# Kernel tuning notes

Hardware: AMD Instinct MI355X
Metric: run time of the kernel (lower is better)

## Reference

```python
import jax, jax.numpy as jnp
import numpy as np

M, N, K, C, G = 16384, 131072, 16, 128, 8
EPS_BN = 1e-5


def _bn(x, g, b):
    # inference-mode BatchNorm1d (running_mean=0, running_var=1)
    return x * (g / jnp.sqrt(1.0 + EPS_BN)) + b


def setup_inputs() -> dict:
    key = jax.random.key(0)
    ks = jax.random.split(key, 16)
    f32 = jnp.float32
    s = 0.05
    return {
        "query_feat": jax.random.normal(ks[0], (M, C), f32),
        "context_feat": jax.random.normal(ks[1], (N, C), f32),
        "query_coord": jax.random.normal(ks[2], (M, 3), f32),
        "context_coord": jax.random.normal(ks[3], (N, 3), f32),
        "Wq": jax.random.normal(ks[4], (C, C), f32) * s,
        "bq": jnp.zeros((C,), f32),
        "gq": jnp.ones((C,), f32),
        "betaq": jnp.zeros((C,), f32),
        "Wk": jax.random.normal(ks[5], (C, C), f32) * s,
        "bk": jnp.zeros((C,), f32),
        "gk": jnp.ones((C,), f32),
        "betak": jnp.zeros((C,), f32),
        "Wv": jax.random.normal(ks[6], (C, C), f32) * s,
        "bv": jnp.zeros((C,), f32),
        "Wp1": jax.random.normal(ks[7], (3, C), f32) * s,
        "bp1": jnp.zeros((C,), f32),
        "gp1": jnp.ones((C,), f32),
        "betap1": jnp.zeros((C,), f32),
        "Wp2": jax.random.normal(ks[8], (C, C), f32) * s,
        "bp2": jnp.zeros((C,), f32),
        "Ww1": jax.random.normal(ks[9], (C, G), f32) * s,
        "bw1": jnp.zeros((G,), f32),
        "gw1": jnp.ones((G,), f32),
        "betaw1": jnp.zeros((G,), f32),
        "Ww2": jax.random.normal(ks[10], (G, G), f32) * s,
        "bw2": jnp.zeros((G,), f32),
        "knn_indexes": jax.random.randint(ks[11], (M, K), 0, N, dtype=jnp.int32),
    }


def reference(query_feat, context_feat, query_coord, context_coord,
              Wq, bq, gq, betaq, Wk, bk, gk, betak, Wv, bv,
              Wp1, bp1, gp1, betap1, Wp2, bp2,
              Ww1, bw1, gw1, betaw1, Ww2, bw2, knn_indexes):
    q = jax.nn.relu(_bn(query_feat @ Wq + bq, gq, betaq))              # (M, C)
    k = jax.nn.relu(_bn(context_feat @ Wk + bk, gk, betak))            # (N, C)
    v = context_feat @ Wv + bv                                         # (N, C)

    mask = knn_indexes >= 0                                            # (M, K); -1 = padded neighbor
    idx = jnp.where(mask, knn_indexes, 0)
    mf = mask[..., None].astype(q.dtype)                               # (M, K, 1)

    key_g = k[idx] * mf                                                # (M, K, C) gather (zero row for -1)
    val_g = v[idx] * mf                                                # (M, K, C)
    pos = (context_coord[idx] - query_coord[:, None, :]) * mf          # (M, K, 3) relative position

    # positional-encoding bias branch (pe_bias=True, pe_multiplier=False)
    peb = jax.nn.relu(_bn(pos @ Wp1 + bp1, gp1, betap1)) @ Wp2 + bp2   # (M, K, C)
    rel = key_g - q[:, None, :] + peb                                  # (M, K, C)
    val_g = val_g + peb

    # grouped vector attention weights
    w = jax.nn.relu(_bn(rel @ Ww1 + bw1, gw1, betaw1)) @ Ww2 + bw2     # (M, K, G)
    w = jax.nn.softmax(w, axis=1) * mf                                 # softmax over neighbors, mask padded

    m_, k_ = idx.shape
    c_ = q.shape[-1]
    g_ = w.shape[-1]
    out = jnp.einsum('mkgi,mkg->mgi', val_g.reshape(m_, k_, g_, c_ // g_), w)
    return out.reshape(m_, c_)
```

## Files before the change

kernel.cpp:

```cpp
#include <hip/hip_runtime.h>

#define C 128
#define G 8
#define KNN 16
#define QB 4
#define EPS 1e-5f

typedef unsigned short u16;
typedef __attribute__((ext_vector_type(8))) short short8;
typedef __attribute__((ext_vector_type(4))) float float4v;

union frag_u { short8 v; u16 u[8]; unsigned d[4]; };

__device__ inline u16 f2bf(float f) {
    unsigned u = __builtin_bit_cast(unsigned, f);
    unsigned r = (u + 0x7fffu + ((u >> 16) & 1u)) >> 16;
    return (u16)r;
}
__device__ inline float bf2f(u16 h) {
    unsigned u = ((unsigned)h) << 16;
    return __builtin_bit_cast(float, u);
}
__device__ inline unsigned pk2(float lo, float hi) {
    unsigned r;
    asm("v_cvt_pk_bf16_f32 %0, %1, %2" : "=v"(r) : "v"(lo), "v"(hi));
    return r;
}
__device__ inline u16 f2bf1(float f) { return (u16)pk2(f, f); }
__device__ inline float bflo(unsigned v) { return __builtin_bit_cast(float, v << 16); }
__device__ inline float bfhi(unsigned v) { return __builtin_bit_cast(float, v & 0xffff0000u); }

__global__ __launch_bounds__(256) void prep_w(
    const float* __restrict__ Wk, const float* __restrict__ Wv,
    const float* __restrict__ Wq, const float* __restrict__ Wp2,
    const float* __restrict__ Ww1, const float* __restrict__ bp2,
    u16* __restrict__ dst, float* __restrict__ cw1)
{
    __shared__ float w1s[C * G];
    const int b = blockIdx.x, t = threadIdx.x;
    if (b < 16) {
        const int mi = b >> 2, qt = b & 3;
        const float* W = mi == 0 ? Wk : mi == 1 ? Wv : mi == 2 ? Wq : Wp2;
        u16* d = dst + mi * 16384;
        for (int e = qt * 4096 + t; e < (qt + 1) * 4096; e += 256) {
            const int k = e >> 7, n = e & 127;
            const int cb = n >> 4, lan = n & 15;
            const int kk = k >> 5, quad = (k >> 3) & 3, j = k & 7;
            d[(((cb * 4 + kk) * 4 + quad) * 16 + lan) * 8 + j] = f2bf(W[e]);
        }
    } else if (b == 16) {
        u16* d = dst + 4 * 16384;
        for (int e = t; e < 4096; e += 256) {
            const int j = e & 7, lan = (e >> 3) & 15;
            const int quad = (e >> 7) & 3, kk = e >> 9;
            const int k = kk * 32 + quad * 8 + j;
            d[e] = lan < 8 ? f2bf(Ww1[k * G + lan]) : (u16)0;
        }
    } else {
        u16* d = dst + 4 * 16384 + 4096;
        for (int e = t; e < 4096; e += 256) d[e] = 0;
        for (int e = t; e < C * G; e += 256) w1s[e] = Ww1[e];
        __syncthreads();
#pragma unroll
        for (int it = 0; it < 4; it++) {
            const int k = it * 32 + (t >> 3), g = t & 7;
            const float4* Wr = (const float4*)(Wp2 + k * C);
            float a = 0.f;
#pragma unroll 8
            for (int i4 = 0; i4 < 32; i4++) {
                const float4 wv = Wr[i4];
                a = fmaf(wv.x, w1s[(i4 * 4 + 0) * G + g], a);
                a = fmaf(wv.y, w1s[(i4 * 4 + 1) * G + g], a);
                a = fmaf(wv.z, w1s[(i4 * 4 + 2) * G + g], a);
                a = fmaf(wv.w, w1s[(i4 * 4 + 3) * G + g], a);
            }
            const int kk = k >> 5, quad = (k >> 3) & 3, j = k & 7;
            d[((kk * 4 + quad) * 16 + g) * 8 + j] = f2bf(a);
        }
        if (t < G) {
            float a = 0.f;
#pragma unroll 8
            for (int i = 0; i < C; i++) a = fmaf(bp2[i], w1s[i * G + t], a);
            cw1[t] = a;
        }
    }
}

__global__ __launch_bounds__(256) void proj_all(
    const float* __restrict__ Xc, const float* __restrict__ Xq,
    const u16* __restrict__ PWk, const float* __restrict__ bk,
    const float* __restrict__ gk, const float* __restrict__ betak,
    const u16* __restrict__ PWv, const float* __restrict__ bv,
    const u16* __restrict__ PWq, const float* __restrict__ bq,
    const float* __restrict__ gq, const float* __restrict__ betaq,
    const u16* __restrict__ PWw1b,
    u16* __restrict__ vout, u16* __restrict__ Kp, u16* __restrict__ Qp,
    int nkv)
{
    __shared__ u16 Xs[64 * 136];
    const int t = threadIdx.x;
    const int w = t >> 6, l = t & 63;
    const int quad = l >> 4, lan = l & 15;
    const bool isq = (int)blockIdx.x >= nkv;
    const long long row0 = (long long)(isq ? blockIdx.x - nkv : blockIdx.x) * 64;
    const float* X = isq ? Xq : Xc;

    {
        const float4* Xv = (const float4*)(X + row0 * C);
#pragma unroll
        for (int i = 0; i < 8; i++) {
            const int e = t + 256 * i;
            const int r = e >> 5, c4 = e & 31;
            const float4 f = Xv[e];
            uint2 p;
            p.x = pk2(f.x, f.y);
            p.y = pk2(f.z, f.w);
            *(uint2*)(&Xs[r * 136 + c4 * 4]) = p;
        }
    }
    __syncthreads();

    if (!isq) {
        unsigned vp[2][4][2];
        {
            short8 Bf[2][4];
#pragma unroll
            for (int ct = 0; ct < 2; ct++) {
                const int cb = w * 2 + ct;
#pragma unroll
                for (int kk = 0; kk < 4; kk++)
                    Bf[ct][kk] = *(const short8*)(PWv + (((cb * 4 + kk) * 4 + quad) * 16 + lan) * 8);
            }
            const float b0v = bv[w * 32 + lan], b1v = bv[w * 32 + 16 + lan];
            float4v acc[2][4];
#pragma unroll
            for (int rt = 0; rt < 4; rt++) {
                acc[0][rt] = (float4v)b0v;
                acc[1][rt] = (float4v)b1v;
            }
#pragma unroll
            for (int rt = 0; rt < 4; rt++)
#pragma unroll
                for (int kk = 0; kk < 4; kk++) {
                    const short8 A = *(const short8*)(&Xs[(rt * 16 + lan) * 136 + kk * 32 + quad * 8]);
#pragma unroll
                    for (int ct = 0; ct < 2; ct++)
                        acc[ct][rt] = __builtin_amdgcn_mfma_f32_16x16x32_bf16(
                            A, Bf[ct][kk], acc[ct][rt], 0, 0, 0);
                }
#pragma unroll
            for (int ct = 0; ct < 2; ct++)
#pragma unroll
                for (int rt = 0; rt < 4; rt++)
#pragma unroll
                    for (int h = 0; h < 2; h++)
                        vp[ct][rt][h] = pk2(acc[ct][rt][2 * h], acc[ct][rt][2 * h + 1]);
        }
        float4v acck[2][4];
        {
            short8 Bf[2][4];
#pragma unroll
            for (int ct = 0; ct < 2; ct++) {
                const int cb = w * 2 + ct;
#pragma unroll
                for (int kk = 0; kk < 4; kk++)
                    Bf[ct][kk] = *(const short8*)(PWk + (((cb * 4 + kk) * 4 + quad) * 16 + lan) * 8);
            }
            const float b0k = bk[w * 32 + lan], b1k = bk[w * 32 + 16 + lan];
#pragma unroll
            for (int rt = 0; rt < 4; rt++) {
                acck[0][rt] = (float4v)b0k;
                acck[1][rt] = (float4v)b1k;
            }
#pragma unroll
            for (int rt = 0; rt < 4; rt++)
#pragma unroll
                for (int kk = 0; kk < 4; kk++) {
                    const short8 A = *(const short8*)(&Xs[(rt * 16 + lan) * 136 + kk * 32 + quad * 8]);
#pragma unroll
                    for (int ct = 0; ct < 2; ct++)
                        acck[ct][rt] = __builtin_amdgcn_mfma_f32_16x16x32_bf16(
                            A, Bf[ct][kk], acck[ct][rt], 0, 0, 0);
                }
        }
        __syncthreads();

#pragma unroll
        for (int ct = 0; ct < 2; ct++) {
            const int cg = w * 32 + ct * 16 + lan;
            const float sc = gk[cg] * rsqrtf(1.f + EPS);
            const float sh = betak[cg];
#pragma unroll
            for (int rt = 0; rt < 4; rt++)
#pragma unroll
                for (int reg = 0; reg < 4; reg++) {
                    float y = fmaf(acck[ct][rt][reg], sc, sh);
                    y = y > 0.f ? y : 0.f;
                    Xs[(rt * 16 + quad * 4 + reg) * 136 + cg] = f2bf1(y);
                }
        }
        __syncthreads();

        {
            short8 Bw[4];
#pragma unroll
            for (int kk = 0; kk < 4; kk++)
                Bw[kk] = *(const short8*)(PWw1b + ((kk * 4 + quad) * 16 + lan) * 8);
            float4v ka = (float4v)0.f;
#pragma unroll
            for (int kk = 0; kk < 4; kk++) {
                const short8 A = *(const short8*)(&Xs[(w * 16 + lan) * 136 + kk * 32 + quad * 8]);
                ka = __builtin_amdgcn_mfma_f32_16x16x32_bf16(A, Bw[kk], ka, 0, 0, 0);
            }
            if (lan < G) {
#pragma unroll
                for (int reg = 0; reg < 4; reg++)
                    Kp[(row0 + w * 16 + quad * 4 + reg) * G + lan] = f2bf1(ka[reg]);
            }
        }
        __syncthreads();

#pragma unroll
        for (int ct = 0; ct < 2; ct++) {
            const int cg = w * 32 + ct * 16 + lan;
#pragma unroll
            for (int rt = 0; rt < 4; rt++)
#pragma unroll
                for (int h = 0; h < 2; h++) {
                    Xs[(rt * 16 + quad * 4 + 2 * h) * 136 + cg]     = (u16)(vp[ct][rt][h] & 0xffffu);
                    Xs[(rt * 16 + quad * 4 + 2 * h + 1) * 136 + cg] = (u16)(vp[ct][rt][h] >> 16);
                }
        }
        __syncthreads();
#pragma unroll
        for (int i = 0; i < 4; i++) {
            const int e = t + 256 * i;
            const int r = e >> 4, cc = (e & 15) * 8;
            *(short8*)(vout + (row0 + r) * C + cc) = *(const short8*)(&Xs[r * 136 + cc]);
        }
    } else {
        float4v acc[2][4];
        {
            short8 Bf[2][4];
#pragma unroll
            for (int ct = 0; ct < 2; ct++) {
                const int cb = w * 2 + ct;
#pragma unroll
                for (int kk = 0; kk < 4; kk++)
                    Bf[ct][kk] = *(const short8*)(PWq + (((cb * 4 + kk) * 4 + quad) * 16 + lan) * 8);
            }
            const float b0q = bq[w * 32 + lan], b1q = bq[w * 32 + 16 + lan];
#pragma unroll
            for (int rt = 0; rt < 4; rt++) {
                acc[0][rt] = (float4v)b0q;
                acc[1][rt] = (float4v)b1q;
            }
#pragma unroll
            for (int rt = 0; rt < 4; rt++)
#pragma unroll
                for (int kk = 0; kk < 4; kk++) {
                    const short8 A = *(const short8*)(&Xs[(rt * 16 + lan) * 136 + kk * 32 + quad * 8]);
#pragma unroll
                    for (int ct = 0; ct < 2; ct++)
                        acc[ct][rt] = __builtin_amdgcn_mfma_f32_16x16x32_bf16(
                            A, Bf[ct][kk], acc[ct][rt], 0, 0, 0);
                }
        }
        __syncthreads();
#pragma unroll
        for (int ct = 0; ct < 2; ct++) {
            const int cg = w * 32 + ct * 16 + lan;
            const float sc = gq[cg] * rsqrtf(1.f + EPS);
            const float sh = betaq[cg];
#pragma unroll
            for (int rt = 0; rt < 4; rt++)
#pragma unroll
                for (int reg = 0; reg < 4; reg++) {
                    float y = fmaf(acc[ct][rt][reg], sc, sh);
                    y = y > 0.f ? y : 0.f;
                    Xs[(rt * 16 + quad * 4 + reg) * 136 + cg] = f2bf1(y);
                }
        }
        __syncthreads();
        {
            short8 Bw[4];
#pragma unroll
            for (int kk = 0; kk < 4; kk++)
                Bw[kk] = *(const short8*)(PWw1b + ((kk * 4 + quad) * 16 + lan) * 8);
            float4v qa = (float4v)0.f;
#pragma unroll
            for (int kk = 0; kk < 4; kk++) {
                const short8 A = *(const short8*)(&Xs[(w * 16 + lan) * 136 + kk * 32 + quad * 8]);
                qa = __builtin_amdgcn_mfma_f32_16x16x32_bf16(A, Bw[kk], qa, 0, 0, 0);
            }
            if (lan < G) {
#pragma unroll
                for (int reg = 0; reg < 4; reg++)
                    Qp[(row0 + w * 16 + quad * 4 + reg) * G + lan] = f2bf1(qa[reg]);
            }
        }
    }
}

__global__ __launch_bounds__(256) void attn6(
    const u16* __restrict__ vbuf, const u16* __restrict__ Kp,
    const u16* __restrict__ Qp,
    const float* __restrict__ qcoord, const float* __restrict__ ccoord,
    const float* __restrict__ Wp1, const float* __restrict__ bp1,
    const float* __restrict__ gp1, const float* __restrict__ betap1,
    const u16* __restrict__ PWp2, const float* __restrict__ bp2,
    const u16* __restrict__ PWp2pb, const float* __restrict__ cw1,
    const float* __restrict__ bw1,
    const float* __restrict__ gw1, const float* __restrict__ betaw1,
    const float* __restrict__ Ww2, const float* __restrict__ bw2,
    const int* __restrict__ knn, float* __restrict__ out)
{
    __shared__ u16   fA[64 * 136];
    __shared__ u16   kgs[64 * G];
    __shared__ float qps[QB * G];
    __shared__ float pebp[64 * G];
    __shared__ float cw1s[G];
    __shared__ float ww2s[G * G];
    __shared__ float pxs[64], pys[64], pzs[64];
    __shared__ int   idxs[64];
    __shared__ float wl[QB * 16 * G];

    const int t = threadIdx.x;
    const int w = t >> 6, l = t & 63;
    const int quad = l >> 4, lan = l & 15;
    const int m0 = blockIdx.x * QB;
    const int rsub = t >> 4;
    const int c8 = (t & 15) * 8;

    float mfr[4];
    frag_u vg[4];
#pragma unroll
    for (int p = 0; p < 4; p++) {
        const int ii = knn[m0 * KNN + p * 16 + rsub];
        mfr[p] = ii >= 0 ? 1.f : 0.f;
        const size_t i0 = ii >= 0 ? ii : 0;
        vg[p].v = *(const short8*)(vbuf + i0 * C + c8);
    }
    if (t < 64) {
        const int q = t >> 4;
        const int ii = knn[m0 * KNN + t];
        const float mf = ii >= 0 ? 1.f : 0.f;
        const int i0 = ii >= 0 ? ii : 0;
        idxs[t] = ii;
        pxs[t] = (ccoord[i0 * 3 + 0] - qcoord[(m0 + q) * 3 + 0]) * mf;
        pys[t] = (ccoord[i0 * 3 + 1] - qcoord[(m0 + q) * 3 + 1]) * mf;
        pzs[t] = (ccoord[i0 * 3 + 2] - qcoord[(m0 + q) * 3 + 2]) * mf;
        *(short8*)(&kgs[t * G]) = *(const short8*)(Kp + (size_t)i0 * G);
    } else if (t < 68) {
        const int p = t - 64;
        frag_u qv;
        qv.v = *(const short8*)(Qp + (size_t)(m0 + p) * G);
#pragma unroll
        for (int j = 0; j < G; j++) qps[p * G + j] = bf2f(qv.u[j]);
    } else if (t < 76) {
        cw1s[t - 68] = cw1[t - 68];
    } else if (t < 76 + G * G) {
        ww2s[t - 76] = Ww2[t - 76];
    }
    __syncthreads();

    {
        const int pc = t & 63;
        const int c0 = 2 * pc;
        const float2 g2  = *(const float2*)(&gp1[c0]);
        const float2 b2  = *(const float2*)(&bp1[c0]);
        const float2 be2 = *(const float2*)(&betap1[c0]);
        const float2 wr0 = *(const float2*)(&Wp1[c0]);
        const float2 wr1 = *(const float2*)(&Wp1[C + c0]);
        const float2 wr2 = *(const float2*)(&Wp1[2 * C + c0]);
        const float rsq = rsqrtf(1.f + EPS);
        const float sc0 = g2.x * rsq, sc1 = g2.y * rsq;
        const float w00 = wr0.x * sc0, w01 = wr0.y * sc1;
        const float w10 = wr1.x * sc0, w11 = wr1.y * sc1;
        const float w20 = wr2.x * sc0, w21 = wr2.y * sc1;
        const float bb0 = fmaf(b2.x, sc0, be2.x);
        const float bb1 = fmaf(b2.y, sc1, be2.y);
#pragma unroll
        for (int r2 = 0; r2 < 16; r2++) {
            const int r = w * 16 + r2;
            const float x = pxs[r], y = pys[r], z = pzs[r];
            float ya = fmaf(x, w00, fmaf(y, w10, fmaf(z, w20, bb0)));
            float yb = fmaf(x, w01, fmaf(y, w11, fmaf(z, w21, bb1)));
            ya = ya > 0.f ? ya : 0.f;
            yb = yb > 0.f ? yb : 0.f;
            *(unsigned*)(&fA[r * 136 + c0]) = pk2(ya, yb);
        }
    }
    __syncthreads();

    float4v acc[2][4];
    float4v pp = (float4v)0.f;
    {
        short8 Bf[2][4];
#pragma unroll
        for (int ct = 0; ct < 2; ct++) {
            const int cb = w * 2 + ct;
#pragma unroll
            for (int kk = 0; kk < 4; kk++)
                Bf[ct][kk] = *(const short8*)(PWp2 + (((cb * 4 + kk) * 4 + quad) * 16 + lan) * 8);
        }
        const float b0 = bp2[w * 32 + lan], b1 = bp2[w * 32 + 16 + lan];
#pragma unroll
        for (int q = 0; q < 4; q++) {
            acc[0][q] = (float4v)b0;
            acc[1][q] = (float4v)b1;
        }
#pragma unroll
        for (int q = 0; q < 4; q++)
#pragma unroll
            for (int kk = 0; kk < 4; kk++) {
                const short8 A = *(const short8*)(&fA[(q * 16 + lan) * 136 + kk * 32 + quad * 8]);
#pragma unroll
                for (int ct = 0; ct < 2; ct++)
                    acc[ct][q] = __builtin_amdgcn_mfma_f32_16x16x32_bf16(
                        A, Bf[ct][kk], acc[ct][q], 0, 0, 0);
            }
#pragma unroll
        for (int kk = 0; kk < 4; kk++) {
            const short8 Bp = *(const short8*)(PWp2pb + ((kk * 4 + quad) * 16 + lan) * 8);
            const short8 A = *(const short8*)(&fA[(w * 16 + lan) * 136 + kk * 32 + quad * 8]);
            pp = __builtin_amdgcn_mfma_f32_16x16x32_bf16(A, Bp, pp, 0, 0, 0);
        }
    }
    __syncthreads();

    {
#pragma unroll
        for (int ct = 0; ct < 2; ct++)
#pragma unroll
            for (int q = 0; q < 4; q++)
#pragma unroll
                for (int reg = 0; reg < 4; reg++)
                    fA[(q * 16 + quad * 4 + reg) * 136 + w * 32 + ct * 16 + lan] =
                        f2bf1(acc[ct][q][reg]);
        if (lan < G) {
#pragma unroll
            for (int reg = 0; reg < 4; reg++)
                pebp[(w * 16 + quad * 4 + reg) * G + lan] = pp[reg];
        }
    }
    __syncthreads();

    {
#pragma unroll
        for (int p = 0; p < 4; p++) {
            const int r = p * 16 + rsub;
            const float mf = mfr[p];
            frag_u peb, o;
            peb.v = *(const short8*)(&fA[r * 136 + c8]);
#pragma unroll
            for (int dd = 0; dd < 4; dd++) {
                const unsigned pv = peb.d[dd], vv = vg[p].d[dd];
                o.d[dd] = pk2(fmaf(bflo(vv), mf, bflo(pv)),
                              fmaf(bfhi(vv), mf, bfhi(pv)));
            }
            *(short8*)(&fA[r * 136 + c8]) = o.v;
        }
    }
    {
        const int j = l & 15;
        const int r = (w << 4) + j;
        const float mf = idxs[r] >= 0 ? 1.f : 0.f;
        const int g0 = 2 * quad, g1 = g0 + 1;
        const float L0 = bf2f(kgs[r * G + g0]) * mf - qps[w * G + g0]
                       + pebp[r * G + g0] + cw1s[g0] + bw1[g0];
        const float L1 = bf2f(kgs[r * G + g1]) * mf - qps[w * G + g1]
                       + pebp[r * G + g1] + cw1s[g1] + bw1[g1];
        const float y0 = L0 * (gw1[g0] * rsqrtf(1.f + EPS)) + betaw1[g0];
        const float y1 = L1 * (gw1[g1] * rsqrtf(1.f + EPS)) + betaw1[g1];
        wl[w * 128 + j * 8 + g0] = y0 > 0.f ? y0 : 0.f;
        wl[w * 128 + j * 8 + g1] = y1 > 0.f ? y1 : 0.f;
    }
    __syncthreads();

    {
        const int j = l & 15;
        const int g0 = 2 * quad, g1 = g0 + 1;
        float hw_[8];
#pragma unroll
        for (int g = 0; g < 8; g++) hw_[g] = wl[w * 128 + j * 8 + g];
        float a0 = bw2[g0], a1 = bw2[g1];
#pragma unroll
        for (int g = 0; g < 8; g++) {
            a0 = fmaf(hw_[g], ww2s[g * 8 + g0], a0);
            a1 = fmaf(hw_[g], ww2s[g * 8 + g1], a1);
        }
        float mx0 = a0, mx1 = a1;
#pragma unroll
        for (int off = 1; off < 16; off <<= 1) {
            mx0 = fmaxf(mx0, __shfl_xor(mx0, off));
            mx1 = fmaxf(mx1, __shfl_xor(mx1, off));
        }
        const float e0 = __expf(a0 - mx0), e1 = __expf(a1 - mx1);
        float s0 = e0, s1 = e1;
#pragma unroll
        for (int off = 1; off < 16; off <<= 1) {
            s0 += __shfl_xor(s0, off);
            s1 += __shfl_xor(s1, off);
        }
        const float mf = idxs[(w << 4) + j] >= 0 ? 1.f : 0.f;
        wl[w * 128 + j * 8 + g0] = e0 * (1.f / s0) * mf;
        wl[w * 128 + j * 8 + g1] = e1 * (1.f / s1) * mf;
    }
    __syncthreads();

    {
        const int q = t >> 6;
        const int pc = t & 63;
        const int c0 = 2 * pc;
        const int g = pc >> 3;
        float s0 = 0.f, s1 = 0.f;
#pragma unroll
        for (int j = 0; j < KNN; j++) {
            const unsigned v = *(const unsigned*)(&fA[(q * 16 + j) * 136 + c0]);
            const float wv = wl[q * 128 + j * 8 + g];
            s0 = fmaf(bflo(v), wv, s0);
            s1 = fmaf(bfhi(v), wv, s1);
        }
        *(float2*)(&out[(size_t)(m0 + q) * C + c0]) = make_float2(s0, s1);
    }
}

extern "C" void kernel_launch(void* const* d_in, const int* in_sizes, int n_in,
                              void* d_out, int out_size, void* d_ws, size_t ws_size,
                              hipStream_t stream)
{
    const float* query_feat    = (const float*)d_in[0];
    const float* context_feat  = (const float*)d_in[1];
    const float* query_coord   = (const float*)d_in[2];
    const float* context_coord = (const float*)d_in[3];
    const float* Wq    = (const float*)d_in[4];
    const float* bq    = (const float*)d_in[5];
    const float* gq    = (const float*)d_in[6];
    const float* betaq = (const float*)d_in[7];
    const float* Wk    = (const float*)d_in[8];
    const float* bk    = (const float*)d_in[9];
    const float* gk    = (const float*)d_in[10];
    const float* betak = (const float*)d_in[11];
    const float* Wv    = (const float*)d_in[12];
    const float* bv    = (const float*)d_in[13];
    const float* Wp1   = (const float*)d_in[14];
    const float* bp1   = (const float*)d_in[15];
    const float* gp1   = (const float*)d_in[16];
    const float* betap1= (const float*)d_in[17];
    const float* Wp2   = (const float*)d_in[18];
    const float* bp2   = (const float*)d_in[19];
    const float* Ww1   = (const float*)d_in[20];
    const float* bw1   = (const float*)d_in[21];
    const float* gw1   = (const float*)d_in[22];
    const float* betaw1= (const float*)d_in[23];
    const float* Ww2   = (const float*)d_in[24];
    const float* bw2   = (const float*)d_in[25];
    const int*   knn   = (const int*)d_in[26];

    const int M = in_sizes[0] / C;
    const int N = in_sizes[1] / C;

    u16* vb = (u16*)d_ws;
    u16* Kp = vb + (size_t)N * C;
    u16* Qp = Kp + (size_t)N * G;
    u16* pw = Qp + (size_t)M * G;
    u16* pWk    = pw;
    u16* pWv    = pw + 16384;
    u16* pWq    = pw + 2 * 16384;
    u16* pWp2   = pw + 3 * 16384;
    u16* pWw1b  = pw + 4 * 16384;
    u16* pWp2pb = pw + 4 * 16384 + 4096;
    float* cw1  = (float*)(pw + 4 * 16384 + 2 * 4096);

    prep_w<<<18, 256, 0, stream>>>(Wk, Wv, Wq, Wp2, Ww1, bp2, pw, cw1);
    proj_all<<<N / 64 + M / 64, 256, 0, stream>>>(
        context_feat, query_feat,
        pWk, bk, gk, betak, pWv, bv,
        pWq, bq, gq, betaq, pWw1b,
        vb, Kp, Qp, N / 64);
    attn6<<<M / QB, 256, 0, stream>>>(vb, Kp, Qp, query_coord, context_coord,
                                      Wp1, bp1, gp1, betap1, pWp2, bp2,
                                      pWp2pb, cw1, bw1, gw1, betaw1, Ww2, bw2,
                                      knn, (float*)d_out);
}
```

Before: 209.8 us.

## Process eight queries per attention block and pack relative positions as float4

```diff
diff --git a/kernel.cpp b/kernel.cpp
--- a/kernel.cpp
+++ b/kernel.cpp
@@ -3,7 +3,7 @@
 #define C 128
 #define G 8
 #define KNN 16
-#define QB 4
+#define QB 8
 #define EPS 1e-5f
 
 typedef unsigned short u16;
@@ -315,14 +315,14 @@
     const float* __restrict__ Ww2, const float* __restrict__ bw2,
     const int* __restrict__ knn, float* __restrict__ out)
 {
-    __shared__ u16   fA[64 * 136];
-    __shared__ u16   kgs[64 * G];
+    __shared__ u16   fA[128 * 136];
+    __shared__ u16   kgs[128 * G];
     __shared__ float qps[QB * G];
-    __shared__ float pebp[64 * G];
+    __shared__ float pebp[128 * G];
     __shared__ float cw1s[G];
     __shared__ float ww2s[G * G];
-    __shared__ float pxs[64], pys[64], pzs[64];
-    __shared__ int   idxs[64];
+    __shared__ float4 ps4[128];
+    __shared__ int   idxs[128];
     __shared__ float wl[QB * 16 * G];
 
     const int t = threadIdx.x;
@@ -332,35 +332,38 @@
     const int rsub = t >> 4;
     const int c8 = (t & 15) * 8;
 
-    float mfr[4];
-    frag_u vg[4];
-#pragma unroll
-    for (int p = 0; p < 4; p++) {
+    float mfr[8];
+    frag_u vg[8];
+#pragma unroll
+    for (int p = 0; p < 8; p++) {
         const int ii = knn[m0 * KNN + p * 16 + rsub];
         mfr[p] = ii >= 0 ? 1.f : 0.f;
         const size_t i0 = ii >= 0 ? ii : 0;
         vg[p].v = *(const short8*)(vbuf + i0 * C + c8);
     }
-    if (t < 64) {
+    if (t < 128) {
         const int q = t >> 4;
         const int ii = knn[m0 * KNN + t];
         const float mf = ii >= 0 ? 1.f : 0.f;
         const int i0 = ii >= 0 ? ii : 0;
         idxs[t] = ii;
-        pxs[t] = (ccoord[i0 * 3 + 0] - qcoord[(m0 + q) * 3 + 0]) * mf;
-        pys[t] = (ccoord[i0 * 3 + 1] - qcoord[(m0 + q) * 3 + 1]) * mf;
-        pzs[t] = (ccoord[i0 * 3 + 2] - qcoord[(m0 + q) * 3 + 2]) * mf;
+        float4 p4;
+        p4.x = (ccoord[i0 * 3 + 0] - qcoord[(m0 + q) * 3 + 0]) * mf;
+        p4.y = (ccoord[i0 * 3 + 1] - qcoord[(m0 + q) * 3 + 1]) * mf;
+        p4.z = (ccoord[i0 * 3 + 2] - qcoord[(m0 + q) * 3 + 2]) * mf;
+        p4.w = 0.f;
+        ps4[t] = p4;
         *(short8*)(&kgs[t * G]) = *(const short8*)(Kp + (size_t)i0 * G);
-    } else if (t < 68) {
-        const int p = t - 64;
+    } else if (t < 128 + QB) {
+        const int p = t - 128;
         frag_u qv;
         qv.v = *(const short8*)(Qp + (size_t)(m0 + p) * G);
 #pragma unroll
         for (int j = 0; j < G; j++) qps[p * G + j] = bf2f(qv.u[j]);
-    } else if (t < 76) {
-        cw1s[t - 68] = cw1[t - 68];
-    } else if (t < 76 + G * G) {
-        ww2s[t - 76] = Ww2[t - 76];
+    } else if (t < 136 + G) {
+        cw1s[t - 136] = cw1[t - 136];
+    } else if (t < 144 + G * G) {
+        ww2s[t - 144] = Ww2[t - 144];
     }
     __syncthreads();
 
@@ -381,11 +384,11 @@
         const float bb0 = fmaf(b2.x, sc0, be2.x);
         const float bb1 = fmaf(b2.y, sc1, be2.y);
 #pragma unroll
-        for (int r2 = 0; r2 < 16; r2++) {
-            const int r = w * 16 + r2;
-            const float x = pxs[r], y = pys[r], z = pzs[r];
-            float ya = fmaf(x, w00, fmaf(y, w10, fmaf(z, w20, bb0)));
-            float yb = fmaf(x, w01, fmaf(y, w11, fmaf(z, w21, bb1)));
+        for (int r2 = 0; r2 < 32; r2++) {
+            const int r = w * 32 + r2;
+            const float4 p4 = ps4[r];
+            float ya = fmaf(p4.x, w00, fmaf(p4.y, w10, fmaf(p4.z, w20, bb0)));
+            float yb = fmaf(p4.x, w01, fmaf(p4.y, w11, fmaf(p4.z, w21, bb1)));
             ya = ya > 0.f ? ya : 0.f;
             yb = yb > 0.f ? yb : 0.f;
             *(unsigned*)(&fA[r * 136 + c0]) = pk2(ya, yb);
@@ -393,8 +396,8 @@
     }
     __syncthreads();
 
-    float4v acc[2][4];
-    float4v pp = (float4v)0.f;
+    float4v acc[2][8];
+    float4v pp0 = (float4v)0.f, pp1 = (float4v)0.f;
     {
         short8 Bf[2][4];
 #pragma unroll
@@ -406,12 +409,12 @@
         }
         const float b0 = bp2[w * 32 + lan], b1 = bp2[w * 32 + 16 + lan];
 #pragma unroll
-        for (int q = 0; q < 4; q++) {
+        for (int q = 0; q < 8; q++) {
             acc[0][q] = (float4v)b0;
             acc[1][q] = (float4v)b1;
         }
 #pragma unroll
-        for (int q = 0; q < 4; q++)
+        for (int q = 0; q < 8; q++)
 #pragma unroll
             for (int kk = 0; kk < 4; kk++) {
                 const short8 A = *(const short8*)(&fA[(q * 16 + lan) * 136 + kk * 32 + quad * 8]);
@@ -420,11 +423,16 @@
                     acc[ct][q] = __builtin_amdgcn_mfma_f32_16x16x32_bf16(
                         A, Bf[ct][kk], acc[ct][q], 0, 0, 0);
             }
+        short8 Bp[4];
+#pragma unroll
+        for (int kk = 0; kk < 4; kk++)
+            Bp[kk] = *(const short8*)(PWp2pb + ((kk * 4 + quad) * 16 + lan) * 8);
 #pragma unroll
         for (int kk = 0; kk < 4; kk++) {
-            const short8 Bp = *(const short8*)(PWp2pb + ((kk * 4 + quad) * 16 + lan) * 8);
-            const short8 A = *(const short8*)(&fA[(w * 16 + lan) * 136 + kk * 32 + quad * 8]);
-            pp = __builtin_amdgcn_mfma_f32_16x16x32_bf16(A, Bp, pp, 0, 0, 0);
+            const short8 A0 = *(const short8*)(&fA[(w * 16 + lan) * 136 + kk * 32 + quad * 8]);
+            pp0 = __builtin_amdgcn_mfma_f32_16x16x32_bf16(A0, Bp[kk], pp0, 0, 0, 0);
+            const short8 A1 = *(const short8*)(&fA[((w + 4) * 16 + lan) * 136 + kk * 32 + quad * 8]);
+            pp1 = __builtin_amdgcn_mfma_f32_16x16x32_bf16(A1, Bp[kk], pp1, 0, 0, 0);
         }
     }
     __syncthreads();
@@ -433,22 +441,24 @@
 #pragma unroll
         for (int ct = 0; ct < 2; ct++)
 #pragma unroll
-            for (int q = 0; q < 4; q++)
+            for (int q = 0; q < 8; q++)
 #pragma unroll
                 for (int reg = 0; reg < 4; reg++)
                     fA[(q * 16 + quad * 4 + reg) * 136 + w * 32 + ct * 16 + lan] =
                         f2bf1(acc[ct][q][reg]);
         if (lan < G) {
 #pragma unroll
-            for (int reg = 0; reg < 4; reg++)
-                pebp[(w * 16 + quad * 4 + reg) * G + lan] = pp[reg];
+            for (int reg = 0; reg < 4; reg++) {
+                pebp[(w * 16 + quad * 4 + reg) * G + lan] = pp0[reg];
+                pebp[((w + 4) * 16 + quad * 4 + reg) * G + lan] = pp1[reg];
+            }
         }
     }
     __syncthreads();
 
     {
 #pragma unroll
-        for (int p = 0; p < 4; p++) {
+        for (int p = 0; p < 8; p++) {
             const int r = p * 16 + rsub;
             const float mf = mfr[p];
             frag_u peb, o;
@@ -464,65 +474,79 @@
     }
     {
         const int j = l & 15;
-        const int r = (w << 4) + j;
-        const float mf = idxs[r] >= 0 ? 1.f : 0.f;
         const int g0 = 2 * quad, g1 = g0 + 1;
-        const float L0 = bf2f(kgs[r * G + g0]) * mf - qps[w * G + g0]
-                       + pebp[r * G + g0] + cw1s[g0] + bw1[g0];
-        const float L1 = bf2f(kgs[r * G + g1]) * mf - qps[w * G + g1]
-                       + pebp[r * G + g1] + cw1s[g1] + bw1[g1];
-        const float y0 = L0 * (gw1[g0] * rsqrtf(1.f + EPS)) + betaw1[g0];
-        const float y1 = L1 * (gw1[g1] * rsqrtf(1.f + EPS)) + betaw1[g1];
-        wl[w * 128 + j * 8 + g0] = y0 > 0.f ? y0 : 0.f;
-        wl[w * 128 + j * 8 + g1] = y1 > 0.f ? y1 : 0.f;
+        const float scw0 = gw1[g0] * rsqrtf(1.f + EPS);
+        const float scw1 = gw1[g1] * rsqrtf(1.f + EPS);
+#pragma unroll
+        for (int qq = 0; qq < 2; qq++) {
+            const int q = 4 * qq + w;
+            const int r = (q << 4) + j;
+            const float mf = idxs[r] >= 0 ? 1.f : 0.f;
+            const float L0 = bf2f(kgs[r * G + g0]) * mf - qps[q * G + g0]
+                           + pebp[r * G + g0] + cw1s[g0] + bw1[g0];
+            const float L1 = bf2f(kgs[r * G + g1]) * mf - qps[q * G + g1]
+                           + pebp[r * G + g1] + cw1s[g1] + bw1[g1];
+            const float y0 = L0 * scw0 + betaw1[g0];
+            const float y1 = L1 * scw1 + betaw1[g1];
+            wl[q * 128 + j * 8 + g0] = y0 > 0.f ? y0 : 0.f;
+            wl[q * 128 + j * 8 + g1] = y1 > 0.f ? y1 : 0.f;
+        }
     }
     __syncthreads();
 
     {
         const int j = l & 15;
         const int g0 = 2 * quad, g1 = g0 + 1;
-        float hw_[8];
-#pragma unroll
-        for (int g = 0; g < 8; g++) hw_[g] = wl[w * 128 + j * 8 + g];
-        float a0 = bw2[g0], a1 = bw2[g1];
-#pragma unroll
-        for (int g = 0; g < 8; g++) {
-            a0 = fmaf(hw_[g], ww2s[g * 8 + g0], a0);
-            a1 = fmaf(hw_[g], ww2s[g * 8 + g1], a1);
-        }
-        float mx0 = a0, mx1 = a1;
-#pragma unroll
-        for (int off = 1; off < 16; off <<= 1) {
-            mx0 = fmaxf(mx0, __shfl_xor(mx0, off));
-            mx1 = fmaxf(mx1, __shfl_xor(mx1, off));
-        }
-        const float e0 = __expf(a0 - mx0), e1 = __expf(a1 - mx1);
-        float s0 = e0, s1 = e1;
-#pragma unroll
-        for (int off = 1; off < 16; off <<= 1) {
-            s0 += __shfl_xor(s0, off);
-            s1 += __shfl_xor(s1, off);
-        }
-        const float mf = idxs[(w << 4) + j] >= 0 ? 1.f : 0.f;
-        wl[w * 128 + j * 8 + g0] = e0 * (1.f / s0) * mf;
-        wl[w * 128 + j * 8 + g1] = e1 * (1.f / s1) * mf;
+        const float bb0 = bw2[g0], bb1 = bw2[g1];
+#pragma unroll
+        for (int qq = 0; qq < 2; qq++) {
+            const int q = 4 * qq + w;
+            float hw_[8];
+#pragma unroll
+            for (int g = 0; g < 8; g++) hw_[g] = wl[q * 128 + j * 8 + g];
+            float a0 = bb0, a1 = bb1;
+#pragma unroll
+            for (int g = 0; g < 8; g++) {
+                a0 = fmaf(hw_[g], ww2s[g * 8 + g0], a0);
+                a1 = fmaf(hw_[g], ww2s[g * 8 + g1], a1);
+            }
+            float mx0 = a0, mx1 = a1;
+#pragma unroll
+            for (int off = 1; off < 16; off <<= 1) {
+                mx0 = fmaxf(mx0, __shfl_xor(mx0, off));
+                mx1 = fmaxf(mx1, __shfl_xor(mx1, off));
+            }
+            const float e0 = __expf(a0 - mx0), e1 = __expf(a1 - mx1);
+            float s0 = e0, s1 = e1;
+#pragma unroll
+            for (int off = 1; off < 16; off <<= 1) {
+                s0 += __shfl_xor(s0, off);
+                s1 += __shfl_xor(s1, off);
+            }
+            const float mf = idxs[(q << 4) + j] >= 0 ? 1.f : 0.f;
+            wl[q * 128 + j * 8 + g0] = e0 * (1.f / s0) * mf;
+            wl[q * 128 + j * 8 + g1] = e1 * (1.f / s1) * mf;
+        }
     }
     __syncthreads();
 
     {
-        const int q = t >> 6;
         const int pc = t & 63;
         const int c0 = 2 * pc;
         const int g = pc >> 3;
-        float s0 = 0.f, s1 = 0.f;
-#pragma unroll
-        for (int j = 0; j < KNN; j++) {
-            const unsigned v = *(const unsigned*)(&fA[(q * 16 + j) * 136 + c0]);
-            const float wv = wl[q * 128 + j * 8 + g];
-            s0 = fmaf(bflo(v), wv, s0);
-            s1 = fmaf(bfhi(v), wv, s1);
-        }
-        *(float2*)(&out[(size_t)(m0 + q) * C + c0]) = make_float2(s0, s1);
+#pragma unroll
+        for (int qq = 0; qq < 2; qq++) {
+            const int q = 4 * qq + w;
+            float s0 = 0.f, s1 = 0.f;
+#pragma unroll
+            for (int j = 0; j < KNN; j++) {
+                const unsigned v = *(const unsigned*)(&fA[(q * 16 + j) * 136 + c0]);
+                const float wv = wl[q * 128 + j * 8 + g];
+                s0 = fmaf(bflo(v), wv, s0);
+                s1 = fmaf(bfhi(v), wv, s1);
+            }
+            *(float2*)(&out[(size_t)(m0 + q) * C + c0]) = make_float2(s0, s1);
+        }
     }
 }
 
```

After: 209.6 us. Within noise of the previous version (-0.1%).
